# Kernel tuning notes

Hardware: AMD Instinct MI355X
Metric: run time of the kernel (lower is better)

## Reference

```python
import jax, jax.numpy as jnp
import numpy as np

EPS = 1e-6
LN_EPS = 1e-6

def _mlstm_parallel_stabilized(q, k, v, igate_preact, fgate_preact):
    # q,k,v: (B,NH,S,DH); igate_preact,fgate_preact: (B,NH,S,1)
    B, NH, S, DH = q.shape
    log_fg = jax.nn.log_sigmoid(fgate_preact[..., 0])            # (B,NH,S)
    cs = jnp.cumsum(log_fg, axis=-1)                             # (B,NH,S)
    # log decay matrix: entry (i,j) = cumsum_i - cumsum_j, lower-triangular (j<=i)
    fg_mat = cs[..., :, None] - cs[..., None, :]                 # (B,NH,S,S)
    mask = jnp.tril(jnp.ones((S, S), dtype=bool))
    log_D = jnp.where(mask, fg_mat + igate_preact[..., 0][..., None, :], -jnp.inf)
    max_log_D = jnp.max(log_D, axis=-1, keepdims=True)           # (B,NH,S,1)
    D = jnp.exp(log_D - max_log_D)                               # (B,NH,S,S)
    k_scaled = k / jnp.sqrt(jnp.float32(DH)).astype(k.dtype)
    qk = jnp.einsum('bhsd,bhtd->bhst', q, k_scaled)              # (B,NH,S,S)
    C = qk * D
    normalizer = jnp.maximum(jnp.abs(jnp.sum(C, axis=-1, keepdims=True)), jnp.exp(-max_log_D))
    C_norm = C / (normalizer + EPS)
    return jnp.einsum('bhst,bhtd->bhsd', C_norm, v)              # (B,NH,S,DH)

def _multihead_layernorm(x, weight):
    # x: (B,NH,S,DH), weight: (NH,DH); normalize over DH per head, no bias
    mu = jnp.mean(x, axis=-1, keepdims=True)
    var = jnp.mean(jnp.square(x - mu), axis=-1, keepdims=True)
    xn = (x - mu) * jax.lax.rsqrt(var + LN_EPS)
    return xn * weight[None, :, None, :]

def setup_inputs() -> dict:
    key = jax.random.key(0)
    ks = jax.random.split(key, 6)
    B, S, E, NH = 2, 2048, 1024, 8
    q = jax.random.normal(ks[0], (B, S, E), dtype=jnp.float32)
    k = jax.random.normal(ks[1], (B, S, E), dtype=jnp.float32)
    v = jax.random.normal(ks[2], (B, S, E), dtype=jnp.float32)
    igate_kernel = jnp.zeros((3 * E, NH), dtype=jnp.float32)
    igate_bias = 0.1 * jax.random.normal(ks[3], (NH,), dtype=jnp.float32)
    fgate_kernel = jnp.zeros((3 * E, NH), dtype=jnp.float32)
    fgate_bias = jnp.linspace(3.0, 6.0, NH, dtype=jnp.float32)
    outnorm_weight = jnp.ones((NH, E // NH), dtype=jnp.float32)
    return {"q": q, "k": k, "v": v,
            "igate_kernel": igate_kernel, "igate_bias": igate_bias,
            "fgate_kernel": fgate_kernel, "fgate_bias": fgate_bias,
            "outnorm_weight": outnorm_weight}

def reference(q, k, v, igate_kernel, igate_bias, fgate_kernel, fgate_bias, outnorm_weight):
    B, S, E = q.shape
    NH = igate_bias.shape[0]
    qkv = jnp.concatenate([q, k, v], axis=-1)                    # (B,S,3E)
    igate_preact = qkv @ igate_kernel + igate_bias               # (B,S,NH)
    fgate_preact = qkv @ fgate_kernel + fgate_bias               # (B,S,NH)
    qh = q.reshape(B, S, NH, -1).transpose(0, 2, 1, 3)           # (B,NH,S,DH)
    kh = k.reshape(B, S, NH, -1).transpose(0, 2, 1, 3)
    vh = v.reshape(B, S, NH, -1).transpose(0, 2, 1, 3)
    ig = igate_preact.transpose(0, 2, 1)[..., None]              # (B,NH,S,1)
    fg = fgate_preact.transpose(0, 2, 1)[..., None]
    h = _mlstm_parallel_stabilized(qh, kh, vh, ig, fg)           # (B,NH,S,DH)
    h_norm = _multihead_layernorm(h, outnorm_weight)
    return h_norm.transpose(0, 2, 1, 3).reshape(B, S, -1)        # (B,S,E)
```

## Files before the change

kernel.cpp:

```cpp
#include <hip/hip_runtime.h>
#include <math.h>

#define S_LEN 2048
#define E_DIM 1024
#define NHEAD 8
#define DHEAD 128

typedef short bf16x8 __attribute__((ext_vector_type(8)));
typedef float f32x4 __attribute__((ext_vector_type(4)));
typedef unsigned int u32x4 __attribute__((ext_vector_type(4)));
typedef unsigned int u32x2 __attribute__((ext_vector_type(2)));

constexpr float RSQ_DH  = 0.08838834764831843f;
constexpr float LNRSQ   = -2.4260151319598084f;
constexpr float EPS_NORM = 1e-6f;
constexpr float LN_EPS_C = 1e-6f;

__device__ inline unsigned bfpair(float lo, float hi) {
  unsigned a = __builtin_bit_cast(unsigned, lo);
  unsigned b = __builtin_bit_cast(unsigned, hi);
  a = (a + 0x7fffu + ((a >> 16) & 1u)) >> 16;
  b = (b + 0x7fffu + ((b >> 16) & 1u)) >> 16;
  return a | (b << 16);
}

__device__ inline unsigned cvtpk(float lo, float hi) {
  unsigned r;
  asm("v_cvt_pk_bf16_f32 %0, %1, %2" : "=v"(r) : "v"(lo), "v"(hi));
  return r;
}

__device__ inline void gload_lds16(const void* g, void* lds) {
  __builtin_amdgcn_global_load_lds(
      (const __attribute__((address_space(1))) unsigned int*)g,
      (__attribute__((address_space(3))) unsigned int*)lds, 16, 0, 0);
}
__device__ inline void gload_lds4(const void* g, void* lds) {
  __builtin_amdgcn_global_load_lds(
      (const __attribute__((address_space(1))) unsigned int*)g,
      (__attribute__((address_space(3))) unsigned int*)lds, 4, 0, 0);
}

__global__ __launch_bounds__(256) void gates_fused(
    const float* __restrict__ q, const float* __restrict__ k, const float* __restrict__ v,
    const float* __restrict__ Wi, const float* __restrict__ bi,
    const float* __restrict__ Wf, const float* __restrict__ bf,
    float* __restrict__ ig_pre, float* __restrict__ fg_pre,
    unsigned short* __restrict__ kb) {
  const int t = threadIdx.x;
  const int row0 = blockIdx.x * 4;
  const int b = row0 >> 11;
  const int s0 = row0 & 2047;
  float p[4][16];
#pragma unroll
  for (int rr = 0; rr < 4; ++rr)
#pragma unroll
    for (int c = 0; c < 16; ++c) p[rr][c] = 0.f;

#pragma unroll
  for (int i = 0; i < 3; ++i) {
    const float* base = (i == 0) ? q : (i == 1) ? k : v;
    float xs[4][4];
#pragma unroll
    for (int rr = 0; rr < 4; ++rr) {
      const float4 xv = *(const float4*)(base + (size_t)(row0 + rr) * E_DIM + t * 4);
      xs[rr][0] = xv.x; xs[rr][1] = xv.y; xs[rr][2] = xv.z; xs[rr][3] = xv.w;
    }
#pragma unroll
    for (int j = 0; j < 4; ++j) {
      const int ge = i * E_DIM + t * 4 + j;
      const float4 wiA = *(const float4*)(Wi + (size_t)ge * 8);
      const float4 wiB = *(const float4*)(Wi + (size_t)ge * 8 + 4);
      const float4 wfA = *(const float4*)(Wf + (size_t)ge * 8);
      const float4 wfB = *(const float4*)(Wf + (size_t)ge * 8 + 4);
      const float wv16[16] = {wiA.x, wiA.y, wiA.z, wiA.w, wiB.x, wiB.y, wiB.z, wiB.w,
                              wfA.x, wfA.y, wfA.z, wfA.w, wfB.x, wfB.y, wfB.z, wfB.w};
#pragma unroll
      for (int rr = 0; rr < 4; ++rr) {
        const float x = xs[rr][j];
#pragma unroll
        for (int c = 0; c < 16; ++c) p[rr][c] += x * wv16[c];
      }
    }
    if (i == 1 && kb != nullptr) {
      const int h = (t * 4) >> 7, d = (t * 4) & 127;
#pragma unroll
      for (int rr = 0; rr < 4; ++rr) {
        u32x2 pk;
        pk.x = bfpair(xs[rr][0], xs[rr][1]);
        pk.y = bfpair(xs[rr][2], xs[rr][3]);
        *(u32x2*)(kb + (((size_t)b * NHEAD + h) * S_LEN + (s0 + rr)) * DHEAD + d) = pk;
      }
    }
  }

#pragma unroll
  for (int rr = 0; rr < 4; ++rr)
#pragma unroll
    for (int c = 0; c < 16; ++c) {
      float val = p[rr][c];
      val += __shfl_xor(val, 1);
      val += __shfl_xor(val, 2);
      val += __shfl_xor(val, 4);
      val += __shfl_xor(val, 8);
      val += __shfl_xor(val, 16);
      val += __shfl_xor(val, 32);
      p[rr][c] = val;
    }
  __shared__ float sred[4][4][16];
  const int wid = t >> 6, lane = t & 63;
  if (lane == 0) {
#pragma unroll
    for (int rr = 0; rr < 4; ++rr)
#pragma unroll
      for (int c = 0; c < 16; ++c) sred[wid][rr][c] = p[rr][c];
  }
  __syncthreads();
  if (t < 64) {
    const int rr = t >> 4, c = t & 15;
    float sum = sred[0][rr][c] + sred[1][rr][c] + sred[2][rr][c] + sred[3][rr][c];
    const int h = c & 7;
    const int row = row0 + rr;
    const int bb = row / S_LEN, s = row % S_LEN;
    if (c < 8) ig_pre[((size_t)bb * NHEAD + h) * S_LEN + s] = sum + bi[h];
    else       fg_pre[((size_t)bb * NHEAD + h) * S_LEN + s] = sum + bf[h];
  }
}

__global__ __launch_bounds__(256) void vtrans(const float* __restrict__ v,
                                              unsigned short* __restrict__ vtb) {
  __shared__ unsigned int tile[128][36];
  const int bid = blockIdx.x;
  const int bh = bid >> 5, st = bid & 31;
  const int b = bh >> 3, h = bh & 7;
  const int s0 = st * 64;
  const int t = threadIdx.x;
#pragma unroll
  for (int i = 0; i < 4; ++i) {
    const int task = t + 256 * i;
    const int sp = task & 31, dq = task >> 5;
    const float* src = v + ((size_t)b * S_LEN + s0 + 2 * sp) * E_DIM + h * DHEAD + dq * 4;
    const float4 r0 = *(const float4*)(src);
    const float4 r1 = *(const float4*)(src + E_DIM);
    tile[dq * 4 + 0][sp] = bfpair(r0.x, r1.x);
    tile[dq * 4 + 1][sp] = bfpair(r0.y, r1.y);
    tile[dq * 4 + 2][sp] = bfpair(r0.z, r1.z);
    tile[dq * 4 + 3][sp] = bfpair(r0.w, r1.w);
  }
  __syncthreads();
#pragma unroll
  for (int i = 0; i < 2; ++i) {
    const int task = t + 256 * i;
    const int d = task >> 2, c4 = task & 3;
    u32x4 w0, w1;
    w0.x = tile[d][c4 * 8 + 0]; w0.y = tile[d][c4 * 8 + 1];
    w0.z = tile[d][c4 * 8 + 2]; w0.w = tile[d][c4 * 8 + 3];
    w1.x = tile[d][c4 * 8 + 4]; w1.y = tile[d][c4 * 8 + 5];
    w1.z = tile[d][c4 * 8 + 6]; w1.w = tile[d][c4 * 8 + 7];
    unsigned short* dst = vtb + ((size_t)bh * DHEAD + d) * S_LEN + s0 + c4 * 16;
    *(u32x4*)(dst)     = w0;
    *(u32x4*)(dst + 8) = w1;
  }
}

__global__ __launch_bounds__(256) void scan_kernel(
    const float* __restrict__ ig_pre, const float* __restrict__ fg_pre,
    float* __restrict__ cs_out, float* __restrict__ g_out, float* __restrict__ gmax_out,
    float g_add) {
  const int bhh = blockIdx.x;
  const int t = threadIdx.x;
  const int lane = t & 63, wid = t >> 6;
  const size_t base = (size_t)bhh * S_LEN;
  float vals[8];
  float run = 0.f;
#pragma unroll
  for (int i = 0; i < 8; ++i) {
    const float x = fg_pre[base + t * 8 + i];
    const float lf = fminf(x, 0.f) - log1pf(__expf(-fabsf(x)));
    run += lf;
    vals[i] = run;
  }
  float ws = run;
#pragma unroll
  for (int off = 1; off < 64; off <<= 1) {
    const float v = __shfl_up(ws, off);
    if (lane >= off) ws += v;
  }
  __shared__ float wsum[4];
  if (lane == 63) wsum[wid] = ws;
  __syncthreads();
  float wpre = 0.f;
#pragma unroll
  for (int kk = 0; kk < 4; ++kk)
    if (kk < wid) wpre += wsum[kk];
  const float prefix = wpre + (ws - run);

  float g_loc[8], gm_loc[8];
  float lmax = -3.4e38f;
#pragma unroll
  for (int i = 0; i < 8; ++i) {
    const float csv = vals[i] + prefix;
    vals[i] = csv;
    const float gg = ig_pre[base + t * 8 + i] - csv;
    g_loc[i] = gg;
    lmax = fmaxf(lmax, gg);
    gm_loc[i] = lmax;
  }
  float wm = lmax;
#pragma unroll
  for (int off = 1; off < 64; off <<= 1) {
    const float v = __shfl_up(wm, off);
    if (lane >= off) wm = fmaxf(wm, v);
  }
  __shared__ float wmax[4];
  if (lane == 63) wmax[wid] = wm;
  __syncthreads();
  float mpre = -3.4e38f;
#pragma unroll
  for (int kk = 0; kk < 4; ++kk)
    if (kk < wid) mpre = fmaxf(mpre, wmax[kk]);
  float excl = __shfl_up(wm, 1);
  if (lane == 0) excl = -3.4e38f;
  const float pmax = fmaxf(mpre, excl);

#pragma unroll
  for (int i = 0; i < 8; ++i) {
    cs_out[base + t * 8 + i]   = vals[i];
    g_out[base + t * 8 + i]    = g_loc[i] + g_add;
    gmax_out[base + t * 8 + i] = fmaxf(gm_loc[i], pmax);
  }
}

__global__ __launch_bounds__(256) void mlstm_mfma9(
    const unsigned short* __restrict__ kb, const unsigned short* __restrict__ vtb,
    const float* __restrict__ q,
    const float* __restrict__ cs, const float* __restrict__ garr, const float* __restrict__ gmax,
    const float* __restrict__ wgt, float* __restrict__ out) {
  __shared__ __align__(16) unsigned char kbuf[4][8192];
  __shared__ __align__(16) unsigned char vbuf[4][8192];
  __shared__ float g_sh[4][32];
  __shared__ float den_sh[4][64];

  const int bid = blockIdx.x;
  int qb;
  if (bid < 256) qb = 31 - (bid >> 4);
  else           qb = (bid - 256) >> 4;
  const int g16 = bid & 15;
  const int bh = 2 * (g16 & 7) + (g16 >> 3);
  const int b = bh >> 3, h = bh & 7;
  const int t = threadIdx.x;
  const int w = t >> 6;
  const int iw = w & 1;
  const int tp = w >> 1;
  const int l = t & 63;
  const int r = l & 15;
  const int qq = l >> 4;
  const size_t bhS = (size_t)bh * S_LEN;

  const int grA = qb * 64 + 4 * r + 2 * iw;
  const int grB = grA + 1;
  const float gmA = gmax[bhS + grA];
  const float gmB = gmax[bhS + grB];
  const float rAB = __expf(gmA - gmB);

  bf16x8 qfA[4], qfB[4];
  {
    const float* qrowA = q + ((size_t)b * S_LEN + grA) * E_DIM + h * DHEAD;
    const float* qrowB = q + ((size_t)b * S_LEN + grB) * E_DIM + h * DHEAD;
#pragma unroll
    for (int c = 0; c < 4; ++c) {
      float4 f0 = *(const float4*)(qrowA + 32 * c + 8 * qq);
      float4 f1 = *(const float4*)(qrowA + 32 * c + 8 * qq + 4);
      u32x4 u;
      u.x = bfpair(f0.x, f0.y); u.y = bfpair(f0.z, f0.w);
      u.z = bfpair(f1.x, f1.y); u.w = bfpair(f1.z, f1.w);
      qfA[c] = __builtin_bit_cast(bf16x8, u);
      f0 = *(const float4*)(qrowB + 32 * c + 8 * qq);
      f1 = *(const float4*)(qrowB + 32 * c + 8 * qq + 4);
      u.x = bfpair(f0.x, f0.y); u.y = bfpair(f0.z, f0.w);
      u.z = bfpair(f1.x, f1.y); u.w = bfpair(f1.z, f1.w);
      qfB[c] = __builtin_bit_cast(bf16x8, u);
    }
  }

  f32x4 oA[8], oB[8];
#pragma unroll
  for (int n = 0; n < 8; ++n) { oA[n] = (f32x4){0,0,0,0}; oB[n] = (f32x4){0,0,0,0}; }
  float denA = 0.f, denB = 0.f;

  const unsigned short* kt = kb + bhS * DHEAD;
  const unsigned short* vt = vtb + (size_t)bh * DHEAD * S_LEN;

  auto stage = [&](int pair, int set) {
    const int j0 = pair * 64 + tp * 32;
    const int bi = set * 2 + tp;
#pragma unroll
    for (int a = 0; a < 4; ++a) {
      const int m = iw * 256 + a * 64 + l;
      const int u = m ^ ((m >> 4) & 7);
      gload_lds16(kt + ((size_t)(j0 + (u >> 4))) * DHEAD + (u & 15) * 8,
                  &kbuf[bi][(iw * 256 + a * 64) * 16]);
    }
#pragma unroll
    for (int a = 0; a < 4; ++a) {
      const int m = iw * 256 + a * 64 + l;
      const int u = m ^ ((m >> 3) & 7);
      gload_lds16(vt + (size_t)(u >> 2) * S_LEN + j0 + (u & 3) * 8,
                  &vbuf[bi][(iw * 256 + a * 64) * 16]);
    }
    if (l < 32) gload_lds4(garr + bhS + j0 + l, &g_sh[bi][0]);
  };

  auto body = [&](int j0, int bi, bool diag) {
    __builtin_amdgcn_s_setprio(1);
    f32x4 sA0 = {0,0,0,0}, sA1 = {0,0,0,0}, sB0 = {0,0,0,0}, sB1 = {0,0,0,0};
#pragma unroll
    for (int c = 0; c < 4; ++c) {
      const int u0 = ((r)      * 16 + 4 * c + qq) ^ (r & 7);
      const int u1 = ((16 + r) * 16 + 4 * c + qq) ^ (r & 7);
      bf16x8 ka0 = *(const bf16x8*)&kbuf[bi][u0 * 16];
      bf16x8 ka1 = *(const bf16x8*)&kbuf[bi][u1 * 16];
      sA0 = __builtin_amdgcn_mfma_f32_16x16x32_bf16(ka0, qfA[c], sA0, 0, 0, 0);
      sB0 = __builtin_amdgcn_mfma_f32_16x16x32_bf16(ka0, qfB[c], sB0, 0, 0, 0);
      sA1 = __builtin_amdgcn_mfma_f32_16x16x32_bf16(ka1, qfA[c], sA1, 0, 0, 0);
      sB1 = __builtin_amdgcn_mfma_f32_16x16x32_bf16(ka1, qfB[c], sB1, 0, 0, 0);
    }
    __builtin_amdgcn_s_setprio(0);

    unsigned PA0[2], PA1[2], PB0[2], PB1[2];
    {
      float wa[4], wb[4];
#pragma unroll
      for (int m = 0; m < 4; ++m) {
        const int jl = 4 * qq + m;
        const float e = __expf(g_sh[bi][jl] - gmA);
        float a = sA0[m] * e;
        float bq = sB0[m] * e * rAB;
        if (diag) {
          if (j0 + jl > grA) a = 0.f;
          if (j0 + jl > grB) bq = 0.f;
        }
        wa[m] = a; wb[m] = bq; denA += a; denB += bq;
      }
      PA0[0] = cvtpk(wa[0], wa[1]); PA0[1] = cvtpk(wa[2], wa[3]);
      PB0[0] = cvtpk(wb[0], wb[1]); PB0[1] = cvtpk(wb[2], wb[3]);
#pragma unroll
      for (int m = 0; m < 4; ++m) {
        const int jl = 16 + 4 * qq + m;
        const float e = __expf(g_sh[bi][jl] - gmA);
        float a = sA1[m] * e;
        float bq = sB1[m] * e * rAB;
        if (diag) {
          if (j0 + jl > grA) a = 0.f;
          if (j0 + jl > grB) bq = 0.f;
        }
        wa[m] = a; wb[m] = bq; denA += a; denB += bq;
      }
      PA1[0] = cvtpk(wa[0], wa[1]); PA1[1] = cvtpk(wa[2], wa[3]);
      PB1[0] = cvtpk(wb[0], wb[1]); PB1[1] = cvtpk(wb[2], wb[3]);
    }

    unsigned AA[4], AB[4];
#pragma unroll
    for (int m = 0; m < 4; ++m) {
      const int srcl = r + 16 * (2 * (qq & 1) + (m >> 1));
      const unsigned a0 = (unsigned)__shfl((int)PA0[m & 1], srcl);
      const unsigned a1 = (unsigned)__shfl((int)PA1[m & 1], srcl);
      const unsigned b0 = (unsigned)__shfl((int)PB0[m & 1], srcl);
      const unsigned b1 = (unsigned)__shfl((int)PB1[m & 1], srcl);
      AA[m] = (qq < 2) ? a0 : a1;
      AB[m] = (qq < 2) ? b0 : b1;
    }
    u32x4 ua, ub;
    ua.x = AA[0]; ua.y = AA[1]; ua.z = AA[2]; ua.w = AA[3];
    ub.x = AB[0]; ub.y = AB[1]; ub.z = AB[2]; ub.w = AB[3];
    const bf16x8 paA = __builtin_bit_cast(bf16x8, ua);
    const bf16x8 paB = __builtin_bit_cast(bf16x8, ub);

    __builtin_amdgcn_s_setprio(1);
#pragma unroll
    for (int n = 0; n < 8; ++n) {
      const int ud = (16 * n + r) * 4 + qq;
      const int up = ud ^ ((ud >> 3) & 7);
      bf16x8 vb = *(const bf16x8*)&vbuf[bi][up * 16];
      oA[n] = __builtin_amdgcn_mfma_f32_16x16x32_bf16(paA, vb, oA[n], 0, 0, 0);
      oB[n] = __builtin_amdgcn_mfma_f32_16x16x32_bf16(paB, vb, oB[n], 0, 0, 0);
    }
    __builtin_amdgcn_s_setprio(0);
  };

  stage(0, 0);
  for (int p = 0; p < qb; ++p) {
    stage(p + 1, (p + 1) & 1);
    asm volatile("s_waitcnt vmcnt(9)" ::: "memory");
    __builtin_amdgcn_sched_barrier(0);
    __syncthreads();
    body(p * 64 + tp * 32, (p & 1) * 2 + tp, false);
    __syncthreads();
  }
  asm volatile("s_waitcnt vmcnt(0)" ::: "memory");
  __builtin_amdgcn_sched_barrier(0);
  __syncthreads();
  body(qb * 64 + tp * 32, (qb & 1) * 2 + tp, true);

  float* osh = (float*)&kbuf[0][0];
  __syncthreads();
  const int xsw = (r & 7) << 2;
  if (tp == 1) {
#pragma unroll
    for (int n = 0; n < 8; ++n) {
      const int i0 = ((((16 * n + r) * 2 + iw) * 2 + 0) * 16 + 4 * qq) ^ xsw;
      const int i1 = ((((16 * n + r) * 2 + iw) * 2 + 1) * 16 + 4 * qq) ^ xsw;
      *(f32x4*)&osh[i0] = oA[n];
      *(f32x4*)&osh[i1] = oB[n];
    }
    den_sh[iw * 2 + 0][l] = denA;
    den_sh[iw * 2 + 1][l] = denB;
  }
  __syncthreads();
  if (tp == 0) {
    denA += den_sh[iw * 2 + 0][l];
    denB += den_sh[iw * 2 + 1][l];
#pragma unroll
    for (int n = 0; n < 8; ++n) {
      const int i0 = ((((16 * n + r) * 2 + iw) * 2 + 0) * 16 + 4 * qq) ^ xsw;
      const int i1 = ((((16 * n + r) * 2 + iw) * 2 + 1) * 16 + 4 * qq) ^ xsw;
      oA[n] += *(const f32x4*)&osh[i0];
      oB[n] += *(const f32x4*)&osh[i1];
    }

    const float* wrow = wgt + h * DHEAD;
    float wv_n[8];
#pragma unroll
    for (int n = 0; n < 8; ++n) wv_n[n] = wrow[16 * n + r];

#pragma unroll
    for (int fg = 0; fg < 2; ++fg) {
      float den_f = (fg == 0) ? denA : denB;
      den_f += __shfl_xor(den_f, 16);
      den_f += __shfl_xor(den_f, 32);
#pragma unroll
      for (int m = 0; m < 4; ++m) {
        const int iloc = 4 * qq + m;
        const float den_o = __shfl(den_f, iloc);
        const int grow = qb * 64 + 4 * iloc + 2 * iw + fg;
        const float csg = cs[bhS + grow];
        const float gmg = gmax[bhS + grow];
        const float norm = fmaxf(fabsf(den_o), __expf(-(csg + gmg))) + EPS_NORM;
        const float inv = 1.f / norm;
        float hv[8];
        float s1 = 0.f, s2 = 0.f;
#pragma unroll
        for (int n = 0; n < 8; ++n) {
          hv[n] = ((fg == 0) ? oA[n][m] : oB[n][m]) * inv;
          s1 += hv[n]; s2 += hv[n] * hv[n];
        }
        s1 += __shfl_xor(s1, 1); s1 += __shfl_xor(s1, 2);
        s1 += __shfl_xor(s1, 4); s1 += __shfl_xor(s1, 8);
        s2 += __shfl_xor(s2, 1); s2 += __shfl_xor(s2, 2);
        s2 += __shfl_xor(s2, 4); s2 += __shfl_xor(s2, 8);
        const float mu  = s1 * (1.f / 128.f);
        const float var = s2 * (1.f / 128.f) - mu * mu;
        const float rstd = rsqrtf(var + LN_EPS_C);
        float* orow = out + ((size_t)b * S_LEN + grow) * E_DIM + h * DHEAD;
#pragma unroll
        for (int n = 0; n < 8; ++n)
          orow[16 * n + r] = (hv[n] - mu) * rstd * wv_n[n];
      }
    }
  }
}

__global__ __launch_bounds__(256) void mlstm_mfma(
    const float* __restrict__ q, const float* __restrict__ k, const float* __restrict__ v,
    const float* __restrict__ cs, const float* __restrict__ garr, const float* __restrict__ gmax,
    const float* __restrict__ wgt, float* __restrict__ out) {
  __shared__ unsigned short k_lds[32][136];
  __shared__ unsigned int   vt_u32[128][20];
  __shared__ unsigned int   xch[4][16][20];
  __shared__ float          g_sh[32];

  const int bid = blockIdx.x;
  int qt;
  if (bid < 256) qt = 31 - (bid >> 4);
  else           qt = (bid - 256) >> 4;
  const int bh = bid & 15;
  const int b = bh >> 3, h = bh & 7;
  const int t = threadIdx.x;
  const int w = t >> 6;
  const int l = t & 63;
  const int r = l & 15;
  const int qq = l >> 4;
  const size_t bhS = (size_t)bh * S_LEN;

  const int gr = qt * 64 + 4 * r + w;
  const float gm_lane = gmax[bhS + gr];

  bf16x8 qfrag[4];
  {
    const float* qrow = q + ((size_t)b * S_LEN + gr) * E_DIM + h * DHEAD;
#pragma unroll
    for (int c = 0; c < 4; ++c) {
      const float4 f0 = *(const float4*)(qrow + 32 * c + 8 * qq);
      const float4 f1 = *(const float4*)(qrow + 32 * c + 8 * qq + 4);
      u32x4 u;
      u.x = bfpair(f0.x, f0.y); u.y = bfpair(f0.z, f0.w);
      u.z = bfpair(f1.x, f1.y); u.w = bfpair(f1.z, f1.w);
      qfrag[c] = __builtin_bit_cast(bf16x8, u);
    }
  }

  f32x4 o[8];
#pragma unroll
  for (int n = 0; n < 8; ++n) o[n] = (f32x4){0.f, 0.f, 0.f, 0.f};
  float den_p = 0.f;

  const int kj = t >> 3, ks = t & 7;
  const int vjp = t & 15, vds = t >> 4;

  const int ntiles = 2 * qt + 2;
  for (int jt = 0; jt < ntiles; ++jt) {
    const int j0 = jt * 32;
    {
      const float* src = k + ((size_t)b * S_LEN + j0 + kj) * E_DIM + h * DHEAD + ks * 16;
      float4 f0 = *(const float4*)(src);
      float4 f1 = *(const float4*)(src + 4);
      float4 f2 = *(const float4*)(src + 8);
      float4 f3 = *(const float4*)(src + 12);
      u32x4 ua, ub;
      ua.x = bfpair(f0.x, f0.y); ua.y = bfpair(f0.z, f0.w);
      ua.z = bfpair(f1.x, f1.y); ua.w = bfpair(f1.z, f1.w);
      ub.x = bfpair(f2.x, f2.y); ub.y = bfpair(f2.z, f2.w);
      ub.z = bfpair(f3.x, f3.y); ub.w = bfpair(f3.z, f3.w);
      *(u32x4*)&k_lds[kj][ks * 16]     = ua;
      *(u32x4*)&k_lds[kj][ks * 16 + 8] = ub;
    }
    {
      const float* s0 = v + ((size_t)b * S_LEN + j0 + 2 * vjp) * E_DIM + h * DHEAD + vds * 8;
      const float* s1 = s0 + E_DIM;
      float4 a0 = *(const float4*)(s0);
      float4 a1 = *(const float4*)(s0 + 4);
      float4 b0 = *(const float4*)(s1);
      float4 b1 = *(const float4*)(s1 + 4);
      vt_u32[vds * 8 + 0][vjp] = bfpair(a0.x, b0.x);
      vt_u32[vds * 8 + 1][vjp] = bfpair(a0.y, b0.y);
      vt_u32[vds * 8 + 2][vjp] = bfpair(a0.z, b0.z);
      vt_u32[vds * 8 + 3][vjp] = bfpair(a0.w, b0.w);
      vt_u32[vds * 8 + 4][vjp] = bfpair(a1.x, b1.x);
      vt_u32[vds * 8 + 5][vjp] = bfpair(a1.y, b1.y);
      vt_u32[vds * 8 + 6][vjp] = bfpair(a1.z, b1.z);
      vt_u32[vds * 8 + 7][vjp] = bfpair(a1.w, b1.w);
    }
    if (t < 32) g_sh[t] = garr[bhS + j0 + t];
    __syncthreads();

    f32x4 st0 = {0, 0, 0, 0}, st1 = {0, 0, 0, 0};
#pragma unroll
    for (int c = 0; c < 4; ++c) {
      bf16x8 ka0 = *(const bf16x8*)&k_lds[r][32 * c + 8 * qq];
      bf16x8 ka1 = *(const bf16x8*)&k_lds[16 + r][32 * c + 8 * qq];
      st0 = __builtin_amdgcn_mfma_f32_16x16x32_bf16(ka0, qfrag[c], st0, 0, 0, 0);
      st1 = __builtin_amdgcn_mfma_f32_16x16x32_bf16(ka1, qfrag[c], st1, 0, 0, 0);
    }

    const bool diag = (jt >= 2 * qt);
    float wv0[4], wv1[4];
#pragma unroll
    for (int reg = 0; reg < 4; ++reg) {
      const int jl0 = 4 * qq + reg, jl1 = 16 + 4 * qq + reg;
      const float e0 = __expf(g_sh[jl0] - gm_lane);
      const float e1 = __expf(g_sh[jl1] - gm_lane);
      float w0 = st0[reg] * RSQ_DH * e0;
      float w1 = st1[reg] * RSQ_DH * e1;
      if (diag) {
        if (j0 + jl0 > gr) w0 = 0.f;
        if (j0 + jl1 > gr) w1 = 0.f;
      }
      wv0[reg] = w0; wv1[reg] = w1;
      den_p += w0 + w1;
    }

    u32x2 p0, p1;
    p0.x = bfpair(wv0[0], wv0[1]); p0.y = bfpair(wv0[2], wv0[3]);
    p1.x = bfpair(wv1[0], wv1[1]); p1.y = bfpair(wv1[2], wv1[3]);
    *(u32x2*)&xch[w][r][2 * qq]     = p0;
    *(u32x2*)&xch[w][r][8 + 2 * qq] = p1;
    __builtin_amdgcn_wave_barrier();
    bf16x8 pa = *(const bf16x8*)&xch[w][r][4 * qq];
    __builtin_amdgcn_wave_barrier();

#pragma unroll
    for (int n = 0; n < 8; ++n) {
      bf16x8 vb = *(const bf16x8*)&vt_u32[16 * n + r][4 * qq];
      o[n] = __builtin_amdgcn_mfma_f32_16x16x32_bf16(pa, vb, o[n], 0, 0, 0);
    }
    __syncthreads();
  }

  float den_f = den_p;
  den_f += __shfl_xor(den_f, 16);
  den_f += __shfl_xor(den_f, 32);

  const float* wrow = wgt + h * DHEAD;
  float wv_n[8];
#pragma unroll
  for (int n = 0; n < 8; ++n) wv_n[n] = wrow[16 * n + r];

#pragma unroll
  for (int reg = 0; reg < 4; ++reg) {
    const int iloc = 4 * qq + reg;
    const float den_o = __shfl(den_f, iloc);
    const int grow = qt * 64 + 4 * iloc + w;
    const float csg = cs[bhS + grow];
    const float gmg = gmax[bhS + grow];
    const float norm = fmaxf(fabsf(den_o), __expf(-(csg + gmg))) + EPS_NORM;
    const float inv = 1.f / norm;
    float hv[8];
    float s1 = 0.f, s2 = 0.f;
#pragma unroll
    for (int n = 0; n < 8; ++n) {
      hv[n] = o[n][reg] * inv;
      s1 += hv[n]; s2 += hv[n] * hv[n];
    }
    s1 += __shfl_xor(s1, 1); s1 += __shfl_xor(s1, 2);
    s1 += __shfl_xor(s1, 4); s1 += __shfl_xor(s1, 8);
    s2 += __shfl_xor(s2, 1); s2 += __shfl_xor(s2, 2);
    s2 += __shfl_xor(s2, 4); s2 += __shfl_xor(s2, 8);
    const float mu  = s1 * (1.f / 128.f);
    const float var = s2 * (1.f / 128.f) - mu * mu;
    const float rstd = rsqrtf(var + LN_EPS_C);
    float* orow = out + ((size_t)b * S_LEN + grow) * E_DIM + h * DHEAD;
#pragma unroll
    for (int n = 0; n < 8; ++n)
      orow[16 * n + r] = (hv[n] - mu) * rstd * wv_n[n];
  }
}

extern "C" void kernel_launch(void* const* d_in, const int* in_sizes, int n_in,
                              void* d_out, int out_size, void* d_ws, size_t ws_size,
                              hipStream_t stream) {
  (void)in_sizes; (void)n_in; (void)out_size;
  const float* q   = (const float*)d_in[0];
  const float* k   = (const float*)d_in[1];
  const float* v   = (const float*)d_in[2];
  const float* Wi  = (const float*)d_in[3];
  const float* bi  = (const float*)d_in[4];
  const float* Wf  = (const float*)d_in[5];
  const float* bf  = (const float*)d_in[6];
  const float* wgt = (const float*)d_in[7];
  float* out = (float*)d_out;
  float* ws  = (float*)d_ws;
  const int BNS = 2 * NHEAD * S_LEN;
  float* ig_pre = ws;
  float* fg_pre = ws + (size_t)BNS;
  float* cs     = ws + (size_t)2 * BNS;
  float* gv     = ws + (size_t)3 * BNS;
  float* gmaxs  = ws + (size_t)4 * BNS;
  unsigned short* kb  = (unsigned short*)(ws + (size_t)5 * BNS);
  unsigned short* vtb = kb + (size_t)16 * S_LEN * DHEAD;

  const size_t need = (size_t)5 * BNS * 4 + (size_t)2 * 16 * S_LEN * DHEAD * 2;

  if (ws_size >= need) {
    gates_fused<<<1024, 256, 0, stream>>>(q, k, v, Wi, bi, Wf, bf, ig_pre, fg_pre, kb);
    vtrans<<<512, 256, 0, stream>>>(v, vtb);
    scan_kernel<<<16, 256, 0, stream>>>(ig_pre, fg_pre, cs, gv, gmaxs, LNRSQ);
    mlstm_mfma9<<<512, 256, 0, stream>>>(kb, vtb, q, cs, gv, gmaxs, wgt, out);
  } else {
    gates_fused<<<1024, 256, 0, stream>>>(q, k, v, Wi, bi, Wf, bf, ig_pre, fg_pre, nullptr);
    scan_kernel<<<16, 256, 0, stream>>>(ig_pre, fg_pre, cs, gv, gmaxs, 0.0f);
    mlstm_mfma<<<512, 256, 0, stream>>>(q, k, v, cs, gv, gmaxs, wgt, out);
  }
}
```

Measured before the change: 102.1 us.

## Merge gate projection and V transpose into one launch with butterfly reduction

```diff
diff --git a/kernel.cpp b/kernel.cpp
--- a/kernel.cpp
+++ b/kernel.cpp
@@ -11,7 +11,6 @@
 typedef unsigned int u32x4 __attribute__((ext_vector_type(4)));
 typedef unsigned int u32x2 __attribute__((ext_vector_type(2)));
 
-constexpr float RSQ_DH  = 0.08838834764831843f;
 constexpr float LNRSQ   = -2.4260151319598084f;
 constexpr float EPS_NORM = 1e-6f;
 constexpr float LN_EPS_C = 1e-6f;
@@ -41,125 +40,139 @@
       (__attribute__((address_space(3))) unsigned int*)lds, 4, 0, 0);
 }
 
-__global__ __launch_bounds__(256) void gates_fused(
+__global__ __launch_bounds__(256) void pre_fused(
     const float* __restrict__ q, const float* __restrict__ k, const float* __restrict__ v,
     const float* __restrict__ Wi, const float* __restrict__ bi,
     const float* __restrict__ Wf, const float* __restrict__ bf,
     float* __restrict__ ig_pre, float* __restrict__ fg_pre,
-    unsigned short* __restrict__ kb) {
+    unsigned short* __restrict__ kb, unsigned short* __restrict__ vtb) {
+  __shared__ float sred[4][4][16];
+  __shared__ unsigned int tile[128][36];
+
   const int t = threadIdx.x;
-  const int row0 = blockIdx.x * 4;
-  const int b = row0 >> 11;
-  const int s0 = row0 & 2047;
-  float p[4][16];
-#pragma unroll
-  for (int rr = 0; rr < 4; ++rr)
-#pragma unroll
-    for (int c = 0; c < 16; ++c) p[rr][c] = 0.f;
-
-#pragma unroll
-  for (int i = 0; i < 3; ++i) {
-    const float* base = (i == 0) ? q : (i == 1) ? k : v;
-    float xs[4][4];
+  if (blockIdx.x < 1024) {
+    const int row0 = blockIdx.x * 4;
+    const int b = row0 >> 11;
+    const int s0 = row0 & 2047;
+    float p[4][16];
+#pragma unroll
+    for (int rr = 0; rr < 4; ++rr)
+#pragma unroll
+      for (int c = 0; c < 16; ++c) p[rr][c] = 0.f;
+
+#pragma unroll
+    for (int i = 0; i < 3; ++i) {
+      const float* base = (i == 0) ? q : (i == 1) ? k : v;
+      float xs[4][4];
+#pragma unroll
+      for (int rr = 0; rr < 4; ++rr) {
+        const float4 xv = *(const float4*)(base + (size_t)(row0 + rr) * E_DIM + t * 4);
+        xs[rr][0] = xv.x; xs[rr][1] = xv.y; xs[rr][2] = xv.z; xs[rr][3] = xv.w;
+      }
+#pragma unroll
+      for (int j = 0; j < 4; ++j) {
+        const int ge = i * E_DIM + t * 4 + j;
+        const float4 wiA = *(const float4*)(Wi + (size_t)ge * 8);
+        const float4 wiB = *(const float4*)(Wi + (size_t)ge * 8 + 4);
+        const float4 wfA = *(const float4*)(Wf + (size_t)ge * 8);
+        const float4 wfB = *(const float4*)(Wf + (size_t)ge * 8 + 4);
+        const float wv16[16] = {wiA.x, wiA.y, wiA.z, wiA.w, wiB.x, wiB.y, wiB.z, wiB.w,
+                                wfA.x, wfA.y, wfA.z, wfA.w, wfB.x, wfB.y, wfB.z, wfB.w};
+#pragma unroll
+        for (int rr = 0; rr < 4; ++rr) {
+          const float x = xs[rr][j];
+#pragma unroll
+          for (int c = 0; c < 16; ++c) p[rr][c] += x * wv16[c];
+        }
+      }
+      if (i == 1) {
+        const int h = (t * 4) >> 7, d = (t * 4) & 127;
+#pragma unroll
+        for (int rr = 0; rr < 4; ++rr) {
+          u32x2 pk;
+          pk.x = bfpair(xs[rr][0], xs[rr][1]);
+          pk.y = bfpair(xs[rr][2], xs[rr][3]);
+          *(u32x2*)(kb + (((size_t)b * NHEAD + h) * S_LEN + (s0 + rr)) * DHEAD + d) = pk;
+        }
+      }
+    }
+
+    const int lane = t & 63, wid = t >> 6;
+    const int crev = ((lane & 1) << 3) | ((lane & 2) << 1) | ((lane & 4) >> 1) | ((lane & 8) >> 3);
 #pragma unroll
     for (int rr = 0; rr < 4; ++rr) {
-      const float4 xv = *(const float4*)(base + (size_t)(row0 + rr) * E_DIM + t * 4);
-      xs[rr][0] = xv.x; xs[rr][1] = xv.y; xs[rr][2] = xv.z; xs[rr][3] = xv.w;
-    }
-#pragma unroll
-    for (int j = 0; j < 4; ++j) {
-      const int ge = i * E_DIM + t * 4 + j;
-      const float4 wiA = *(const float4*)(Wi + (size_t)ge * 8);
-      const float4 wiB = *(const float4*)(Wi + (size_t)ge * 8 + 4);
-      const float4 wfA = *(const float4*)(Wf + (size_t)ge * 8);
-      const float4 wfB = *(const float4*)(Wf + (size_t)ge * 8 + 4);
-      const float wv16[16] = {wiA.x, wiA.y, wiA.z, wiA.w, wiB.x, wiB.y, wiB.z, wiB.w,
-                              wfA.x, wfA.y, wfA.z, wfA.w, wfB.x, wfB.y, wfB.z, wfB.w};
-#pragma unroll
-      for (int rr = 0; rr < 4; ++rr) {
-        const float x = xs[rr][j];
-#pragma unroll
-        for (int c = 0; c < 16; ++c) p[rr][c] += x * wv16[c];
-      }
-    }
-    if (i == 1 && kb != nullptr) {
-      const int h = (t * 4) >> 7, d = (t * 4) & 127;
-#pragma unroll
-      for (int rr = 0; rr < 4; ++rr) {
-        u32x2 pk;
-        pk.x = bfpair(xs[rr][0], xs[rr][1]);
-        pk.y = bfpair(xs[rr][2], xs[rr][3]);
-        *(u32x2*)(kb + (((size_t)b * NHEAD + h) * S_LEN + (s0 + rr)) * DHEAD + d) = pk;
-      }
-    }
-  }
-
-#pragma unroll
-  for (int rr = 0; rr < 4; ++rr)
-#pragma unroll
-    for (int c = 0; c < 16; ++c) {
-      float val = p[rr][c];
-      val += __shfl_xor(val, 1);
-      val += __shfl_xor(val, 2);
-      val += __shfl_xor(val, 4);
-      val += __shfl_xor(val, 8);
-      val += __shfl_xor(val, 16);
-      val += __shfl_xor(val, 32);
-      p[rr][c] = val;
-    }
-  __shared__ float sred[4][4][16];
-  const int wid = t >> 6, lane = t & 63;
-  if (lane == 0) {
-#pragma unroll
-    for (int rr = 0; rr < 4; ++rr)
-#pragma unroll
-      for (int c = 0; c < 16; ++c) sred[wid][rr][c] = p[rr][c];
-  }
-  __syncthreads();
-  if (t < 64) {
-    const int rr = t >> 4, c = t & 15;
-    float sum = sred[0][rr][c] + sred[1][rr][c] + sred[2][rr][c] + sred[3][rr][c];
-    const int h = c & 7;
-    const int row = row0 + rr;
-    const int bb = row / S_LEN, s = row % S_LEN;
-    if (c < 8) ig_pre[((size_t)bb * NHEAD + h) * S_LEN + s] = sum + bi[h];
-    else       fg_pre[((size_t)bb * NHEAD + h) * S_LEN + s] = sum + bf[h];
-  }
-}
-
-__global__ __launch_bounds__(256) void vtrans(const float* __restrict__ v,
-                                              unsigned short* __restrict__ vtb) {
-  __shared__ unsigned int tile[128][36];
-  const int bid = blockIdx.x;
-  const int bh = bid >> 5, st = bid & 31;
-  const int b = bh >> 3, h = bh & 7;
-  const int s0 = st * 64;
-  const int t = threadIdx.x;
-#pragma unroll
-  for (int i = 0; i < 4; ++i) {
-    const int task = t + 256 * i;
-    const int sp = task & 31, dq = task >> 5;
-    const float* src = v + ((size_t)b * S_LEN + s0 + 2 * sp) * E_DIM + h * DHEAD + dq * 4;
-    const float4 r0 = *(const float4*)(src);
-    const float4 r1 = *(const float4*)(src + E_DIM);
-    tile[dq * 4 + 0][sp] = bfpair(r0.x, r1.x);
-    tile[dq * 4 + 1][sp] = bfpair(r0.y, r1.y);
-    tile[dq * 4 + 2][sp] = bfpair(r0.z, r1.z);
-    tile[dq * 4 + 3][sp] = bfpair(r0.w, r1.w);
-  }
-  __syncthreads();
-#pragma unroll
-  for (int i = 0; i < 2; ++i) {
-    const int task = t + 256 * i;
-    const int d = task >> 2, c4 = task & 3;
-    u32x4 w0, w1;
-    w0.x = tile[d][c4 * 8 + 0]; w0.y = tile[d][c4 * 8 + 1];
-    w0.z = tile[d][c4 * 8 + 2]; w0.w = tile[d][c4 * 8 + 3];
-    w1.x = tile[d][c4 * 8 + 4]; w1.y = tile[d][c4 * 8 + 5];
-    w1.z = tile[d][c4 * 8 + 6]; w1.w = tile[d][c4 * 8 + 7];
-    unsigned short* dst = vtb + ((size_t)bh * DHEAD + d) * S_LEN + s0 + c4 * 16;
-    *(u32x4*)(dst)     = w0;
-    *(u32x4*)(dst + 8) = w1;
+      float* vv = p[rr];
+#pragma unroll
+      for (int i = 0; i < 8; ++i) {
+        const float sel = (lane & 1) ? vv[i] : vv[i + 8];
+        const float rcv = __shfl_xor(sel, 1);
+        vv[i] = ((lane & 1) ? vv[i + 8] : vv[i]) + rcv;
+      }
+#pragma unroll
+      for (int i = 0; i < 4; ++i) {
+        const float sel = (lane & 2) ? vv[i] : vv[i + 4];
+        const float rcv = __shfl_xor(sel, 2);
+        vv[i] = ((lane & 2) ? vv[i + 4] : vv[i]) + rcv;
+      }
+#pragma unroll
+      for (int i = 0; i < 2; ++i) {
+        const float sel = (lane & 4) ? vv[i] : vv[i + 2];
+        const float rcv = __shfl_xor(sel, 4);
+        vv[i] = ((lane & 4) ? vv[i + 2] : vv[i]) + rcv;
+      }
+      {
+        const float sel = (lane & 8) ? vv[0] : vv[1];
+        const float rcv = __shfl_xor(sel, 8);
+        vv[0] = ((lane & 8) ? vv[1] : vv[0]) + rcv;
+      }
+      vv[0] += __shfl_xor(vv[0], 16);
+      vv[0] += __shfl_xor(vv[0], 32);
+    }
+    if (lane < 16) {
+#pragma unroll
+      for (int rr = 0; rr < 4; ++rr) sred[wid][rr][crev] = p[rr][0];
+    }
+    __syncthreads();
+    if (t < 64) {
+      const int rr = t >> 4, c = t & 15;
+      float sum = sred[0][rr][c] + sred[1][rr][c] + sred[2][rr][c] + sred[3][rr][c];
+      const int h = c & 7;
+      const int row = row0 + rr;
+      const int bb = row / S_LEN, s = row % S_LEN;
+      if (c < 8) ig_pre[((size_t)bb * NHEAD + h) * S_LEN + s] = sum + bi[h];
+      else       fg_pre[((size_t)bb * NHEAD + h) * S_LEN + s] = sum + bf[h];
+    }
+  } else {
+    const int bid = blockIdx.x - 1024;
+    const int bh = bid >> 5, st = bid & 31;
+    const int b = bh >> 3, h = bh & 7;
+    const int s0 = st * 64;
+#pragma unroll
+    for (int i = 0; i < 4; ++i) {
+      const int task = t + 256 * i;
+      const int sp = task & 31, dq = task >> 5;
+      const float* src = v + ((size_t)b * S_LEN + s0 + 2 * sp) * E_DIM + h * DHEAD + dq * 4;
+      const float4 r0 = *(const float4*)(src);
+      const float4 r1 = *(const float4*)(src + E_DIM);
+      tile[dq * 4 + 0][sp] = bfpair(r0.x, r1.x);
+      tile[dq * 4 + 1][sp] = bfpair(r0.y, r1.y);
+      tile[dq * 4 + 2][sp] = bfpair(r0.z, r1.z);
+      tile[dq * 4 + 3][sp] = bfpair(r0.w, r1.w);
+    }
+    __syncthreads();
+#pragma unroll
+    for (int i = 0; i < 2; ++i) {
+      const int task = t + 256 * i;
+      const int d = task >> 2, c4 = task & 3;
+      u32x4 w0, w1;
+      w0.x = tile[d][c4 * 8 + 0]; w0.y = tile[d][c4 * 8 + 1];
+      w0.z = tile[d][c4 * 8 + 2]; w0.w = tile[d][c4 * 8 + 3];
+      w1.x = tile[d][c4 * 8 + 4]; w1.y = tile[d][c4 * 8 + 5];
+      w1.z = tile[d][c4 * 8 + 6]; w1.w = tile[d][c4 * 8 + 7];
+      unsigned short* dst = vtb + ((size_t)bh * DHEAD + d) * S_LEN + s0 + c4 * 16;
+      *(u32x4*)(dst)     = w0;
+      *(u32x4*)(dst + 8) = w1;
+    }
   }
 }
 
@@ -471,175 +484,10 @@
   }
 }
 
-__global__ __launch_bounds__(256) void mlstm_mfma(
-    const float* __restrict__ q, const float* __restrict__ k, const float* __restrict__ v,
-    const float* __restrict__ cs, const float* __restrict__ garr, const float* __restrict__ gmax,
-    const float* __restrict__ wgt, float* __restrict__ out) {
-  __shared__ unsigned short k_lds[32][136];
-  __shared__ unsigned int   vt_u32[128][20];
-  __shared__ unsigned int   xch[4][16][20];
-  __shared__ float          g_sh[32];
-
-  const int bid = blockIdx.x;
-  int qt;
-  if (bid < 256) qt = 31 - (bid >> 4);
-  else           qt = (bid - 256) >> 4;
-  const int bh = bid & 15;
-  const int b = bh >> 3, h = bh & 7;
-  const int t = threadIdx.x;
-  const int w = t >> 6;
-  const int l = t & 63;
-  const int r = l & 15;
-  const int qq = l >> 4;
-  const size_t bhS = (size_t)bh * S_LEN;
-
-  const int gr = qt * 64 + 4 * r + w;
-  const float gm_lane = gmax[bhS + gr];
-
-  bf16x8 qfrag[4];
-  {
-    const float* qrow = q + ((size_t)b * S_LEN + gr) * E_DIM + h * DHEAD;
-#pragma unroll
-    for (int c = 0; c < 4; ++c) {
-      const float4 f0 = *(const float4*)(qrow + 32 * c + 8 * qq);
-      const float4 f1 = *(const float4*)(qrow + 32 * c + 8 * qq + 4);
-      u32x4 u;
-      u.x = bfpair(f0.x, f0.y); u.y = bfpair(f0.z, f0.w);
-      u.z = bfpair(f1.x, f1.y); u.w = bfpair(f1.z, f1.w);
-      qfrag[c] = __builtin_bit_cast(bf16x8, u);
-    }
-  }
-
-  f32x4 o[8];
-#pragma unroll
-  for (int n = 0; n < 8; ++n) o[n] = (f32x4){0.f, 0.f, 0.f, 0.f};
-  float den_p = 0.f;
-
-  const int kj = t >> 3, ks = t & 7;
-  const int vjp = t & 15, vds = t >> 4;
-
-  const int ntiles = 2 * qt + 2;
-  for (int jt = 0; jt < ntiles; ++jt) {
-    const int j0 = jt * 32;
-    {
-      const float* src = k + ((size_t)b * S_LEN + j0 + kj) * E_DIM + h * DHEAD + ks * 16;
-      float4 f0 = *(const float4*)(src);
-      float4 f1 = *(const float4*)(src + 4);
-      float4 f2 = *(const float4*)(src + 8);
-      float4 f3 = *(const float4*)(src + 12);
-      u32x4 ua, ub;
-      ua.x = bfpair(f0.x, f0.y); ua.y = bfpair(f0.z, f0.w);
-      ua.z = bfpair(f1.x, f1.y); ua.w = bfpair(f1.z, f1.w);
-      ub.x = bfpair(f2.x, f2.y); ub.y = bfpair(f2.z, f2.w);
-      ub.z = bfpair(f3.x, f3.y); ub.w = bfpair(f3.z, f3.w);
-      *(u32x4*)&k_lds[kj][ks * 16]     = ua;
-      *(u32x4*)&k_lds[kj][ks * 16 + 8] = ub;
-    }
-    {
-      const float* s0 = v + ((size_t)b * S_LEN + j0 + 2 * vjp) * E_DIM + h * DHEAD + vds * 8;
-      const float* s1 = s0 + E_DIM;
-      float4 a0 = *(const float4*)(s0);
-      float4 a1 = *(const float4*)(s0 + 4);
-      float4 b0 = *(const float4*)(s1);
-      float4 b1 = *(const float4*)(s1 + 4);
-      vt_u32[vds * 8 + 0][vjp] = bfpair(a0.x, b0.x);
-      vt_u32[vds * 8 + 1][vjp] = bfpair(a0.y, b0.y);
-      vt_u32[vds * 8 + 2][vjp] = bfpair(a0.z, b0.z);
-      vt_u32[vds * 8 + 3][vjp] = bfpair(a0.w, b0.w);
-      vt_u32[vds * 8 + 4][vjp] = bfpair(a1.x, b1.x);
-      vt_u32[vds * 8 + 5][vjp] = bfpair(a1.y, b1.y);
-      vt_u32[vds * 8 + 6][vjp] = bfpair(a1.z, b1.z);
-      vt_u32[vds * 8 + 7][vjp] = bfpair(a1.w, b1.w);
-    }
-    if (t < 32) g_sh[t] = garr[bhS + j0 + t];
-    __syncthreads();
-
-    f32x4 st0 = {0, 0, 0, 0}, st1 = {0, 0, 0, 0};
-#pragma unroll
-    for (int c = 0; c < 4; ++c) {
-      bf16x8 ka0 = *(const bf16x8*)&k_lds[r][32 * c + 8 * qq];
-      bf16x8 ka1 = *(const bf16x8*)&k_lds[16 + r][32 * c + 8 * qq];
-      st0 = __builtin_amdgcn_mfma_f32_16x16x32_bf16(ka0, qfrag[c], st0, 0, 0, 0);
-      st1 = __builtin_amdgcn_mfma_f32_16x16x32_bf16(ka1, qfrag[c], st1, 0, 0, 0);
-    }
-
-    const bool diag = (jt >= 2 * qt);
-    float wv0[4], wv1[4];
-#pragma unroll
-    for (int reg = 0; reg < 4; ++reg) {
-      const int jl0 = 4 * qq + reg, jl1 = 16 + 4 * qq + reg;
-      const float e0 = __expf(g_sh[jl0] - gm_lane);
-      const float e1 = __expf(g_sh[jl1] - gm_lane);
-      float w0 = st0[reg] * RSQ_DH * e0;
-      float w1 = st1[reg] * RSQ_DH * e1;
-      if (diag) {
-        if (j0 + jl0 > gr) w0 = 0.f;
-        if (j0 + jl1 > gr) w1 = 0.f;
-      }
-      wv0[reg] = w0; wv1[reg] = w1;
-      den_p += w0 + w1;
-    }
-
-    u32x2 p0, p1;
-    p0.x = bfpair(wv0[0], wv0[1]); p0.y = bfpair(wv0[2], wv0[3]);
-    p1.x = bfpair(wv1[0], wv1[1]); p1.y = bfpair(wv1[2], wv1[3]);
-    *(u32x2*)&xch[w][r][2 * qq]     = p0;
-    *(u32x2*)&xch[w][r][8 + 2 * qq] = p1;
-    __builtin_amdgcn_wave_barrier();
-    bf16x8 pa = *(const bf16x8*)&xch[w][r][4 * qq];
-    __builtin_amdgcn_wave_barrier();
-
-#pragma unroll
-    for (int n = 0; n < 8; ++n) {
-      bf16x8 vb = *(const bf16x8*)&vt_u32[16 * n + r][4 * qq];
-      o[n] = __builtin_amdgcn_mfma_f32_16x16x32_bf16(pa, vb, o[n], 0, 0, 0);
-    }
-    __syncthreads();
-  }
-
-  float den_f = den_p;
-  den_f += __shfl_xor(den_f, 16);
-  den_f += __shfl_xor(den_f, 32);
-
-  const float* wrow = wgt + h * DHEAD;
-  float wv_n[8];
-#pragma unroll
-  for (int n = 0; n < 8; ++n) wv_n[n] = wrow[16 * n + r];
-
-#pragma unroll
-  for (int reg = 0; reg < 4; ++reg) {
-    const int iloc = 4 * qq + reg;
-    const float den_o = __shfl(den_f, iloc);
-    const int grow = qt * 64 + 4 * iloc + w;
-    const float csg = cs[bhS + grow];
-    const float gmg = gmax[bhS + grow];
-    const float norm = fmaxf(fabsf(den_o), __expf(-(csg + gmg))) + EPS_NORM;
-    const float inv = 1.f / norm;
-    float hv[8];
-    float s1 = 0.f, s2 = 0.f;
-#pragma unroll
-    for (int n = 0; n < 8; ++n) {
-      hv[n] = o[n][reg] * inv;
-      s1 += hv[n]; s2 += hv[n] * hv[n];
-    }
-    s1 += __shfl_xor(s1, 1); s1 += __shfl_xor(s1, 2);
-    s1 += __shfl_xor(s1, 4); s1 += __shfl_xor(s1, 8);
-    s2 += __shfl_xor(s2, 1); s2 += __shfl_xor(s2, 2);
-    s2 += __shfl_xor(s2, 4); s2 += __shfl_xor(s2, 8);
-    const float mu  = s1 * (1.f / 128.f);
-    const float var = s2 * (1.f / 128.f) - mu * mu;
-    const float rstd = rsqrtf(var + LN_EPS_C);
-    float* orow = out + ((size_t)b * S_LEN + grow) * E_DIM + h * DHEAD;
-#pragma unroll
-    for (int n = 0; n < 8; ++n)
-      orow[16 * n + r] = (hv[n] - mu) * rstd * wv_n[n];
-  }
-}
-
 extern "C" void kernel_launch(void* const* d_in, const int* in_sizes, int n_in,
                               void* d_out, int out_size, void* d_ws, size_t ws_size,
                               hipStream_t stream) {
-  (void)in_sizes; (void)n_in; (void)out_size;
+  (void)in_sizes; (void)n_in; (void)out_size; (void)ws_size;
   const float* q   = (const float*)d_in[0];
   const float* k   = (const float*)d_in[1];
   const float* v   = (const float*)d_in[2];
@@ -659,16 +507,7 @@
   unsigned short* kb  = (unsigned short*)(ws + (size_t)5 * BNS);
   unsigned short* vtb = kb + (size_t)16 * S_LEN * DHEAD;
 
-  const size_t need = (size_t)5 * BNS * 4 + (size_t)2 * 16 * S_LEN * DHEAD * 2;
-
-  if (ws_size >= need) {
-    gates_fused<<<1024, 256, 0, stream>>>(q, k, v, Wi, bi, Wf, bf, ig_pre, fg_pre, kb);
-    vtrans<<<512, 256, 0, stream>>>(v, vtb);
-    scan_kernel<<<16, 256, 0, stream>>>(ig_pre, fg_pre, cs, gv, gmaxs, LNRSQ);
-    mlstm_mfma9<<<512, 256, 0, stream>>>(kb, vtb, q, cs, gv, gmaxs, wgt, out);
-  } else {
-    gates_fused<<<1024, 256, 0, stream>>>(q, k, v, Wi, bi, Wf, bf, ig_pre, fg_pre, nullptr);
-    scan_kernel<<<16, 256, 0, stream>>>(ig_pre, fg_pre, cs, gv, gmaxs, 0.0f);
-    mlstm_mfma<<<512, 256, 0, stream>>>(q, k, v, cs, gv, gmaxs, wgt, out);
-  }
-}
+  pre_fused<<<1536, 256, 0, stream>>>(q, k, v, Wi, bi, Wf, bf, ig_pre, fg_pre, kb, vtb);
+  scan_kernel<<<16, 256, 0, stream>>>(ig_pre, fg_pre, cs, gv, gmaxs, LNRSQ);
+  mlstm_mfma9<<<512, 256, 0, stream>>>(kb, vtb, q, cs, gv, gmaxs, wgt, out);
+}
```

New measurement: 100.7 us. Within noise of the previous version (-1.4%).
